# Optimization experiments

Hardware: AMD Instinct MI355X
Metric: run time of the kernel (lower is better)

## Reference

```python
import jax, jax.numpy as jnp
import numpy as np

D_MODEL = 768
NUM_HEADS = 12
D_K = D_MODEL // NUM_HEADS


def setup_inputs() -> dict:
    key = jax.random.key(0)
    k1, k2, k3 = jax.random.split(key, 3)
    s = 1.0 / np.sqrt(D_MODEL)
    return {
        "x": jax.random.normal(k1, (4, 2048, D_MODEL), dtype=jnp.float32),
        "W_qkv": jax.random.normal(k2, (D_MODEL, 3 * D_MODEL), dtype=jnp.float32) * s,
        "b_qkv": jnp.zeros((3 * D_MODEL,), dtype=jnp.float32),
        "W_out": jax.random.normal(k3, (D_MODEL, D_MODEL), dtype=jnp.float32) * s,
        "b_out": jnp.zeros((D_MODEL,), dtype=jnp.float32),
    }


def reference(x, W_qkv, b_qkv, W_out, b_out):
    B, S, _ = x.shape
    # fused QKV projection: [B,S,3*d_model]
    qkv = x @ W_qkv + b_qkv
    # reshape to [B,S,H,3*d_k] then to [B,H,S,3*d_k] (matches torch permute)
    qkv = qkv.reshape(B, S, NUM_HEADS, 3 * D_K).transpose(0, 2, 1, 3)
    q, k, v = jnp.split(qkv, 3, axis=-1)  # each [B,H,S,d_k]
    scale = 1.0 / jnp.sqrt(jnp.float32(D_K))
    scores = jnp.einsum("bhqd,bhkd->bhqk", q, k) * scale
    attn = jax.nn.softmax(scores, axis=-1)
    context = jnp.einsum("bhqk,bhkd->bhqd", attn, v)
    context = context.transpose(0, 2, 1, 3).reshape(B, S, D_MODEL)
    return context @ W_out + b_out
```

## Files before the change

kernel.cpp:

```cpp
#include <hip/hip_runtime.h>
#include <hip/hip_bf16.h>
#include <math.h>

#define D_MODEL 768
#define NUM_HEADS 12
#define D_K 64
#define SEQ 2048
#define BATCH 4
#define QKV_N 2304

#define QSCALE 0.18033688011112042f
#define MSHIFT 8.0f

typedef _Float16 f16;
typedef f16 f16x4 __attribute__((ext_vector_type(4)));
typedef f16 f16x8 __attribute__((ext_vector_type(8)));
typedef float f32x4 __attribute__((ext_vector_type(4)));

#if __has_builtin(__builtin_amdgcn_exp2f)
#define EXP2F(x) __builtin_amdgcn_exp2f(x)
#else
#define EXP2F(x) __expf(0.6931471805599453f * (x))
#endif

__device__ __forceinline__ void gload_lds16(const f16* g, f16* l) {
  __builtin_amdgcn_global_load_lds(
      (const __attribute__((address_space(1))) void*)g,
      (__attribute__((address_space(3))) void*)l, 16, 0, 0);
}

__device__ inline void xcd_swizzle(int& bx, int& by) {
  const int nx = gridDim.x;
  const int nwg = nx * gridDim.y;
  const int bidlin = blockIdx.y * nx + blockIdx.x;
  const int cpx = nwg >> 3;
  const int wg = (bidlin & 7) * cpx + (bidlin >> 3);
  bx = wg % nx;
  by = wg / nx;
}

__global__ __launch_bounds__(256) void prep_all(
    const float* __restrict__ x, const float* __restrict__ Wq,
    const float* __restrict__ Wo, f16* __restrict__ xh,
    f16* __restrict__ Wqt, f16* __restrict__ Wot) {
  const int bid = blockIdx.x;
  const int tid = threadIdx.x;
  __shared__ f16 t[64][72];

  if (bid < 1536) {
    const int idx = bid * 256 + tid;
#pragma unroll
    for (int i = 0; i < 2; ++i) {
      const size_t c = (size_t)idx + (size_t)i * 393216;
      const float4 a = *(const float4*)(x + c * 8);
      const float4 b = *(const float4*)(x + c * 8 + 4);
      f16x8 h = { (f16)a.x, (f16)a.y, (f16)a.z, (f16)a.w,
                  (f16)b.x, (f16)b.y, (f16)b.z, (f16)b.w };
      *(f16x8*)(xh + c * 8) = h;
    }
    return;
  }

  const float* W;
  f16* Wt;
  int K, N, n0, k0;
  if (bid < 1968) {
    const int tt = bid - 1536;
    W = Wq; Wt = Wqt; K = 768; N = QKV_N;
    n0 = (tt % 36) * 64; k0 = (tt / 36) * 64;
  } else {
    const int tt = bid - 1968;
    W = Wo; Wt = Wot; K = 768; N = D_MODEL;
    n0 = (tt % 12) * 64; k0 = (tt / 12) * 64;
  }

#pragma unroll
  for (int i = 0; i < 4; ++i) {
    const int slot = tid + i * 256;
    const int r = slot >> 4;
    const int c4 = (slot & 15) * 4;
    const float4 v = *(const float4*)(W + (size_t)(k0 + r) * N + n0 + c4);
    t[c4 + 0][r] = (f16)v.x;
    t[c4 + 1][r] = (f16)v.y;
    t[c4 + 2][r] = (f16)v.z;
    t[c4 + 3][r] = (f16)v.w;
  }
  __syncthreads();
#pragma unroll
  for (int i = 0; i < 2; ++i) {
    const int slot = tid + i * 256;
    const int n = slot >> 3;
    const int kc = (slot & 7) * 8;
    *(f16x8*)(Wt + (size_t)(n0 + n) * K + k0 + kc) = *(const f16x8*)(&t[n][kc]);
  }
}

#define GEMM_CORE8(A_, B_, K_)                                              \
  __shared__ f16 Als[128 * 32];                                             \
  __shared__ f16 Bls[128 * 32];                                             \
  f32x4 acc[4][2];                                                          \
  _Pragma("unroll") for (int i = 0; i < 4; ++i)                             \
      _Pragma("unroll") for (int j = 0; j < 2; ++j)                         \
          acc[i][j] = (f32x4){0.f, 0.f, 0.f, 0.f};                          \
  const int srow = w * 16 + (lane >> 2);                                    \
  const int sc8 = (lane & 3) * 8;                                           \
  const f16* gA = A_ + (size_t)(bm + srow) * K_ + sc8;                      \
  const f16* gB = B_ + (size_t)(bn + srow) * K_ + sc8;                      \
  f16* lA = Als + (w * 16) * 32;                                            \
  f16* lB = Bls + (w * 16) * 32;                                            \
  for (int k0 = 0; k0 < K_; k0 += 32) {                                     \
    gload_lds16(gA + k0, lA);                                               \
    gload_lds16(gB + k0, lB);                                               \
    __syncthreads();                                                        \
    f16x8 af[4], bf[2];                                                     \
    _Pragma("unroll") for (int mi = 0; mi < 4; ++mi)                        \
        af[mi] = *(const f16x8*)(Als + (wr * 64 + mi * 16 + c) * 32 + g * 8); \
    _Pragma("unroll") for (int nj = 0; nj < 2; ++nj)                        \
        bf[nj] = *(const f16x8*)(Bls + (wc * 32 + nj * 16 + c) * 32 + g * 8); \
    _Pragma("unroll") for (int mi = 0; mi < 4; ++mi)                        \
        _Pragma("unroll") for (int nj = 0; nj < 2; ++nj)                    \
            acc[mi][nj] = __builtin_amdgcn_mfma_f32_16x16x32_f16(           \
                af[mi], bf[nj], acc[mi][nj], 0, 0, 0);                      \
    __syncthreads();                                                        \
  }

__global__ __launch_bounds__(512, 4) void gemm_qkv(
    const f16* __restrict__ A, const f16* __restrict__ B,
    const float* __restrict__ bias,
    f16* __restrict__ Qh, f16* __restrict__ Kh, f16* __restrict__ Vt) {
  int bx, by;
  xcd_swizzle(bx, by);
  const int bm = by * 128;
  const int bn = bx * 128;
  const int tid = threadIdx.x;
  const int lane = tid & 63;
  const int w = tid >> 6;
  const int wr = w >> 2;
  const int wc = w & 3;
  const int c = lane & 15;
  const int g = lane >> 4;

  GEMM_CORE8(A, B, 768)

  const int crow = g * 4;
#pragma unroll
  for (int nj = 0; nj < 2; ++nj) {
    const int col = bn + wc * 32 + nj * 16 + c;
    const int h = col / 192;
    const int rem = col - h * 192;
    const int sub = rem >> 6;
    const int d = rem & 63;
    const float bv = bias[col];
#pragma unroll
    for (int mi = 0; mi < 4; ++mi) {
      const int tok0 = bm + wr * 64 + mi * 16 + crow;
      const int b = tok0 >> 11;
      const int t0 = tok0 & 2047;
      const int bh = b * NUM_HEADS + h;
      if (sub == 2) {
        f16x4 pv = { (f16)(acc[mi][nj][0] + bv), (f16)(acc[mi][nj][1] + bv),
                     (f16)(acc[mi][nj][2] + bv), (f16)(acc[mi][nj][3] + bv) };
        *(f16x4*)(Vt + ((size_t)bh * 64 + d) * SEQ + t0) = pv;
      } else if (sub == 0) {
#pragma unroll
        for (int r = 0; r < 4; ++r)
          Qh[((size_t)bh * SEQ + t0 + r) * 64 + d] =
              (f16)((acc[mi][nj][r] + bv) * QSCALE);
      } else {
#pragma unroll
        for (int r = 0; r < 4; ++r)
          Kh[((size_t)bh * SEQ + t0 + r) * 64 + d] =
              (f16)(acc[mi][nj][r] + bv);
      }
    }
  }
}

__global__ __launch_bounds__(512, 4) void gemm_out(
    const f16* __restrict__ A, const f16* __restrict__ B,
    const float* __restrict__ bias, float* __restrict__ C) {
  int bx, by;
  xcd_swizzle(bx, by);
  const int bm = by * 128;
  const int bn = bx * 128;
  const int tid = threadIdx.x;
  const int lane = tid & 63;
  const int w = tid >> 6;
  const int wr = w >> 2;
  const int wc = w & 3;
  const int c = lane & 15;
  const int g = lane >> 4;

  GEMM_CORE8(A, B, 768)

  const int crow = g * 4;
#pragma unroll
  for (int nj = 0; nj < 2; ++nj) {
    const int col = bn + wc * 32 + nj * 16 + c;
    const float bv = bias[col];
#pragma unroll
    for (int mi = 0; mi < 4; ++mi) {
      const int rbase = bm + wr * 64 + mi * 16 + crow;
#pragma unroll
      for (int r = 0; r < 4; ++r) {
        C[(size_t)(rbase + r) * D_MODEL + col] = acc[mi][nj][r] + bv;
      }
    }
  }
}

__global__ __launch_bounds__(512, 6) void flash_attn_mfma(
    const f16* __restrict__ Qh, const f16* __restrict__ Kh,
    const f16* __restrict__ Vt, f16* __restrict__ ctxh) {
  const int i = blockIdx.x;
  const int j = i >> 3;
  const int bh = (i & 7) + 8 * (j >> 4);
  const int qt = j & 15;
  const int b = bh / NUM_HEADS;
  const int h = bh - b * NUM_HEADS;
  const int q0 = qt * 128;
  const int tid = threadIdx.x;
  const int lane = tid & 63;
  const int w = tid >> 6;
  const int c = lane & 15;
  const int g = lane >> 4;

  __shared__ f16 Ql[128 * 64];
  __shared__ f16 Kl[64 * 64];
  __shared__ f16 Vl[64 * 64];
  __shared__ f16 Pl[8][16 * 64];

  const f16* Kbase = Kh + (size_t)bh * SEQ * 64;
  const f16* Vbase = Vt + (size_t)bh * 64 * SEQ;

#pragma unroll
  for (int ii = 0; ii < 2; ++ii) {
    const int slot = tid + ii * 512;
    const int row = slot >> 3;
    const int g8 = (slot & 7) * 8;
    f16x8 hq = *(const f16x8*)(Qh + ((size_t)bh * SEQ + q0 + row) * 64 + g8);
    *(f16x8*)(Ql + row * 64 + (g8 ^ ((row & 7) << 3))) = hq;
  }
  {
    const int row = tid >> 3;
    const int g8 = (tid & 7) * 8;
    f16x8 hk = *(const f16x8*)(Kbase + (size_t)row * 64 + g8);
    *(f16x8*)(Kl + row * 64 + (g8 ^ ((row & 7) << 3))) = hk;
    f16x8 hv = *(const f16x8*)(Vbase + (size_t)row * SEQ + g8);
    *(f16x8*)(Vl + row * 64 + (g8 ^ ((row & 7) << 3))) = hv;
  }
  __syncthreads();

  f16x8 qf[2];
#pragma unroll
  for (int s = 0; s < 2; ++s) {
    const int row = w * 16 + c;
    qf[s] = *(const f16x8*)(Ql + row * 64 +
                            ((s * 32 + g * 8) ^ ((row & 7) << 3)));
  }

  f32x4 o[4];
  float lsum = 0.f;
#pragma unroll
  for (int dt = 0; dt < 4; ++dt) o[dt] = (f32x4){0.f, 0.f, 0.f, 0.f};

  const int srow = tid >> 3;
  const int sg8 = (tid & 7) * 8;

  for (int kt = 0; kt < SEQ / 64; ++kt) {
    f16x8 nk, nv;
    const bool more = (kt + 1) < SEQ / 64;
    if (more) {
      nk = *(const f16x8*)(Kbase + (size_t)(kt + 1) * 64 * 64 +
                           (size_t)srow * 64 + sg8);
      nv = *(const f16x8*)(Vbase + (size_t)srow * SEQ + (kt + 1) * 64 + sg8);
    }

    f32x4 s_[4];
#pragma unroll
    for (int mt = 0; mt < 4; ++mt) s_[mt] = (f32x4){0.f, 0.f, 0.f, 0.f};

    __builtin_amdgcn_s_setprio(1);
#pragma unroll
    for (int s2 = 0; s2 < 2; ++s2) {
#pragma unroll
      for (int mt = 0; mt < 4; ++mt) {
        const int row = mt * 16 + c;
        const f16x8 kf = *(const f16x8*)(Kl + row * 64 +
                         ((s2 * 32 + g * 8) ^ ((row & 7) << 3)));
        s_[mt] = __builtin_amdgcn_mfma_f32_16x16x32_f16(
            kf, qf[s2], s_[mt], 0, 0, 0);
      }
    }
    __builtin_amdgcn_s_setprio(0);

    {
#pragma unroll
      for (int mt = 0; mt < 4; ++mt) {
        f32x4 e;
#pragma unroll
        for (int r = 0; r < 4; ++r) {
          e[r] = EXP2F(s_[mt][r] - MSHIFT);
          lsum += e[r];
        }
        s_[mt] = e;
      }

      const int prow = c;
#pragma unroll
      for (int mt = 0; mt < 4; ++mt) {
        f16x4 pk = { (f16)s_[mt][0], (f16)s_[mt][1],
                     (f16)s_[mt][2], (f16)s_[mt][3] };
        *(f16x4*)(&Pl[w][prow * 64 +
                         ((mt * 16 + g * 4) ^ ((prow & 7) << 3))]) = pk;
      }
    }

    __builtin_amdgcn_s_setprio(1);
#pragma unroll
    for (int s2 = 0; s2 < 2; ++s2) {
      const f16x8 pf = *(const f16x8*)(&Pl[w][c * 64 +
                        ((s2 * 32 + g * 8) ^ ((c & 7) << 3))]);
#pragma unroll
      for (int dt = 0; dt < 4; ++dt) {
        const int row = dt * 16 + c;
        const f16x8 vf = *(const f16x8*)(Vl + row * 64 +
                         ((s2 * 32 + g * 8) ^ ((row & 7) << 3)));
        o[dt] = __builtin_amdgcn_mfma_f32_16x16x32_f16(
            vf, pf, o[dt], 0, 0, 0);
      }
    }
    __builtin_amdgcn_s_setprio(0);

    __syncthreads();

    if (more) {
      *(f16x8*)(Kl + srow * 64 + (sg8 ^ ((srow & 7) << 3))) = nk;
      *(f16x8*)(Vl + srow * 64 + (sg8 ^ ((srow & 7) << 3))) = nv;
    }
    __syncthreads();
  }

  {
    float l_ = lsum;
    l_ += __shfl_xor(l_, 16);
    l_ += __shfl_xor(l_, 32);
    const float inv = 1.f / l_;
    const int q = q0 + w * 16 + c;
#pragma unroll
    for (int dt = 0; dt < 4; ++dt) {
      f16x4 r4 = { (f16)(o[dt][0] * inv), (f16)(o[dt][1] * inv),
                   (f16)(o[dt][2] * inv), (f16)(o[dt][3] * inv) };
      *(f16x4*)(ctxh + ((size_t)(b * SEQ) + q) * D_MODEL + h * 64 +
                dt * 16 + g * 4) = r4;
    }
  }
}

extern "C" void kernel_launch(void* const* d_in, const int* in_sizes, int n_in,
                              void* d_out, int out_size, void* d_ws, size_t ws_size,
                              hipStream_t stream) {
  const float* x     = (const float*)d_in[0];
  const float* W_qkv = (const float*)d_in[1];
  const float* b_qkv = (const float*)d_in[2];
  const float* W_out = (const float*)d_in[3];
  const float* b_out = (const float*)d_in[4];
  float* out = (float*)d_out;

  const int M = BATCH * SEQ;
  const int BH = BATCH * NUM_HEADS;

  f16* xh   = (f16*)d_ws;
  f16* Wqt  = xh + (size_t)M * D_MODEL;
  f16* Wot  = Wqt + (size_t)QKV_N * D_MODEL;
  f16* Qh   = Wot + (size_t)D_MODEL * D_MODEL;
  f16* Kh   = Qh + (size_t)BH * SEQ * 64;
  f16* Vt   = Kh + (size_t)BH * SEQ * 64;
  f16* ctxh = Vt + (size_t)BH * SEQ * 64;

  hipLaunchKernelGGL(prep_all, dim3(2112), dim3(256), 0, stream,
                     x, W_qkv, W_out, xh, Wqt, Wot);

  hipLaunchKernelGGL(gemm_qkv, dim3(QKV_N / 128, M / 128), dim3(512), 0,
                     stream, xh, Wqt, b_qkv, Qh, Kh, Vt);

  hipLaunchKernelGGL(flash_attn_mfma, dim3(16 * NUM_HEADS * BATCH),
                     dim3(512), 0, stream, Qh, Kh, Vt, ctxh);

  hipLaunchKernelGGL(gemm_out, dim3(D_MODEL / 128, M / 128), dim3(512), 0,
                     stream, ctxh, Wot, b_out, out);
}
```

Before: 156.1 us.

## Double GEMM K-tile to 64 with XOR-swizzled LDS layout

The shared GEMM core now stages a 64-wide K slice per iteration instead of 32, which halves the number of barrier pairs per output tile. The LDS layout uses an XOR swizzle of the 8-element column chunk by row, applied both when the global loads write LDS and when fragments are read, to avoid bank conflicts on the wider rows. In exchange it doubles LDS use per block, which may reduce occupancy at 512 threads with 4 blocks per CU.

```diff
diff --git a/kernel.cpp b/kernel.cpp
--- a/kernel.cpp
+++ b/kernel.cpp
@@ -96,31 +96,48 @@
 }
 
 #define GEMM_CORE8(A_, B_, K_)                                              \
-  __shared__ f16 Als[128 * 32];                                             \
-  __shared__ f16 Bls[128 * 32];                                             \
+  __shared__ f16 Als[128 * 64];                                             \
+  __shared__ f16 Bls[128 * 64];                                             \
   f32x4 acc[4][2];                                                          \
   _Pragma("unroll") for (int i = 0; i < 4; ++i)                             \
       _Pragma("unroll") for (int j = 0; j < 2; ++j)                         \
           acc[i][j] = (f32x4){0.f, 0.f, 0.f, 0.f};                          \
-  const int srow = w * 16 + (lane >> 2);                                    \
-  const int sc8 = (lane & 3) * 8;                                           \
-  const f16* gA = A_ + (size_t)(bm + srow) * K_ + sc8;                      \
-  const f16* gB = B_ + (size_t)(bn + srow) * K_ + sc8;                      \
-  f16* lA = Als + (w * 16) * 32;                                            \
-  f16* lB = Bls + (w * 16) * 32;                                            \
-  for (int k0 = 0; k0 < K_; k0 += 32) {                                     \
-    gload_lds16(gA + k0, lA);                                               \
-    gload_lds16(gB + k0, lB);                                               \
+  const int sch = lane & 7;                  \
+  const int srw = lane >> 3;                     \
+  const int scol = ((sch ^ srw) * 8);        \
+  const int r0 = w * 16 + srw;                                              \
+  const int r1 = r0 + 8;                           \
+  const f16* gA0 = A_ + (size_t)(bm + r0) * K_ + scol;                      \
+  const f16* gA1 = A_ + (size_t)(bm + r1) * K_ + scol;                      \
+  const f16* gB0 = B_ + (size_t)(bn + r0) * K_ + scol;                      \
+  const f16* gB1 = B_ + (size_t)(bn + r1) * K_ + scol;                      \
+  f16* lA0 = Als + (w * 16) * 64;                                           \
+  f16* lA1 = Als + (w * 16 + 8) * 64;                                       \
+  f16* lB0 = Bls + (w * 16) * 64;                                           \
+  f16* lB1 = Bls + (w * 16 + 8) * 64;                                       \
+  for (int k0 = 0; k0 < K_; k0 += 64) {                                     \
+    gload_lds16(gA0 + k0, lA0);                                             \
+    gload_lds16(gA1 + k0, lA1);                                             \
+    gload_lds16(gB0 + k0, lB0);                                             \
+    gload_lds16(gB1 + k0, lB1);                                             \
     __syncthreads();                                                        \
-    f16x8 af[4], bf[2];                                                     \
-    _Pragma("unroll") for (int mi = 0; mi < 4; ++mi)                        \
-        af[mi] = *(const f16x8*)(Als + (wr * 64 + mi * 16 + c) * 32 + g * 8); \
-    _Pragma("unroll") for (int nj = 0; nj < 2; ++nj)                        \
-        bf[nj] = *(const f16x8*)(Bls + (wc * 32 + nj * 16 + c) * 32 + g * 8); \
-    _Pragma("unroll") for (int mi = 0; mi < 4; ++mi)                        \
-        _Pragma("unroll") for (int nj = 0; nj < 2; ++nj)                    \
-            acc[mi][nj] = __builtin_amdgcn_mfma_f32_16x16x32_f16(           \
-                af[mi], bf[nj], acc[mi][nj], 0, 0, 0);                      \
+    _Pragma("unroll") for (int cc = 0; cc < 2; ++cc) {                      \
+      f16x8 af[4], bf[2];                                                   \
+      _Pragma("unroll") for (int mi = 0; mi < 4; ++mi) {                    \
+        const int row = wr * 64 + mi * 16 + c;                              \
+        af[mi] = *(const f16x8*)(Als + row * 64 +                           \
+                                 ((cc * 4 + g) ^ (row & 7)) * 8);           \
+      }                                                                     \
+      _Pragma("unroll") for (int nj = 0; nj < 2; ++nj) {                    \
+        const int row = wc * 32 + nj * 16 + c;                              \
+        bf[nj] = *(const f16x8*)(Bls + row * 64 +                           \
+                                 ((cc * 4 + g) ^ (row & 7)) * 8);           \
+      }                                                                     \
+      _Pragma("unroll") for (int mi = 0; mi < 4; ++mi)                      \
+          _Pragma("unroll") for (int nj = 0; nj < 2; ++nj)                  \
+              acc[mi][nj] = __builtin_amdgcn_mfma_f32_16x16x32_f16(         \
+                  af[mi], bf[nj], acc[mi][nj], 0, 0, 0);                    \
+    }                                                                       \
     __syncthreads();                                                        \
   }
 
```

Result: faster. 148.2 us, median of 3 (-5.1%).
